# Kernel optimization log

Hardware: AMD Instinct MI355X
Metric: run time of the kernel (lower is better)

Reference implementation:

```python
import jax, jax.numpy as jnp
from jax import lax
import numpy as np

B, H, W, C, N = 4, 512, 512, 32, 300000
K, S, P, D = 3, 2, 1, 1  # kernel, stride, padding, dilation


def setup_inputs() -> dict:
    key = jax.random.key(0)
    kf, _ = jax.random.split(key)
    features = jax.random.normal(kf, (N, C), dtype=jnp.float32)
    # unique active coordinates (spconv requires unique sites)
    rng = np.random.default_rng(0)
    lin = rng.choice(B * H * W, size=N, replace=False)
    b = lin // (H * W)
    y = (lin // W) % H
    x = lin % W
    coors = jnp.asarray(np.stack([b, y, x], axis=1), dtype=jnp.int32)  # [N,3]
    return {"features": features, "coors": coors, "batch_size": B}


def reference(features, coors, batch_size):
    # Scatter active features onto a dense grid initialized to -inf so that
    # inputs only; outputs with no active input in window are inactive).
    neg_inf = jnp.array(-jnp.inf, dtype=features.dtype)
    dense = jnp.full((batch_size, H, W, features.shape[1]), neg_inf,
                     dtype=features.dtype)
    b, y, x = coors[:, 0], coors[:, 1], coors[:, 2]
    dense = dense.at[b, y, x].set(features)  # coords are unique
    out = lax.reduce_window(
        dense, neg_inf, lax.max,
        window_dimensions=(1, K, K, 1),
        window_strides=(1, S, S, 1),
        padding=((0, 0), (P, P), (P, P), (0, 0)),
        window_dilation=(1, D, D, 1))
    # inactive output sites -> 0 (dense view of the sparse output tensor)
    return jnp.where(jnp.isinf(out), jnp.zeros((), out.dtype), out)
```

## Files before the change

kernel.cpp:

```cpp
#include <hip/hip_runtime.h>
#include <math.h>

#define BB 4
#define HH 512
#define WW 512
#define CC 32
#define HO 256
#define WO 256

__global__ void fill_zero_kernel(int4* __restrict__ g, int n4) {
    int i = blockIdx.x * blockDim.x + threadIdx.x;
    if (i < n4) g[i] = make_int4(0, 0, 0, 0);
}

__global__ void scatter_idx_kernel(const int* __restrict__ coors,
                                   int* __restrict__ grid, int n) {
    int i = blockIdx.x * blockDim.x + threadIdx.x;
    if (i >= n) return;
    int b = coors[i * 3 + 0];
    int y = coors[i * 3 + 1];
    int x = coors[i * 3 + 2];
    grid[((size_t)b * HH + y) * WW + x] = i + 1;
}

__global__ void __launch_bounds__(256)
pool_kernel(const float4* __restrict__ feat,
            const int* __restrict__ grid,
            float4* __restrict__ out) {
    int ox_base = (blockIdx.x & 7) * 32;
    int oy      = (blockIdx.x >> 3) & (HO - 1);
    int b       = blockIdx.x >> 11;

    int tid = threadIdx.x;
    int cg  = tid & 7;
    int p   = tid >> 3;

    int iy0 = 2 * oy - 1;
    int gx0 = 2 * ox_base - 1;
    const int* gb = grid + (size_t)b * (HH * WW);

    __shared__ int sg[3 * 66];

    if (tid < 195) {
        int r = tid / 65;
        int c = tid - r * 65;
        int iy = iy0 + r;
        int gx = gx0 + c;
        int v = 0;
        if ((unsigned)iy < (unsigned)HH && (unsigned)gx < (unsigned)WW)
            v = gb[iy * WW + gx];
        sg[r * 66 + c] = v;
    }
    __syncthreads();

    const float NEG = -INFINITY;
    float4 acc = make_float4(NEG, NEG, NEG, NEG);
    int lc = 2 * p;

#pragma unroll
    for (int dy = 0; dy < 3; ++dy) {
#pragma unroll
        for (int dx = 0; dx < 3; ++dx) {
            int v = sg[dy * 66 + lc + dx];
            if (v != 0) {
                float4 f = feat[(size_t)(v - 1) * 8 + cg];
                acc.x = fmaxf(acc.x, f.x);
                acc.y = fmaxf(acc.y, f.y);
                acc.z = fmaxf(acc.z, f.z);
                acc.w = fmaxf(acc.w, f.w);
            }
        }
    }

    acc.x = isinf(acc.x) ? 0.0f : acc.x;
    acc.y = isinf(acc.y) ? 0.0f : acc.y;
    acc.z = isinf(acc.z) ? 0.0f : acc.z;
    acc.w = isinf(acc.w) ? 0.0f : acc.w;

    int pos = ((b * HO + oy) * WO + ox_base + p);
    out[(size_t)pos * 8 + cg] = acc;
}

extern "C" void kernel_launch(void* const* d_in, const int* in_sizes, int n_in,
                              void* d_out, int out_size, void* d_ws, size_t ws_size,
                              hipStream_t stream) {
    const float* features = (const float*)d_in[0];
    const int*   coors    = (const int*)d_in[1];
    int n = in_sizes[0] / CC;

    int* grid = (int*)d_ws;

    {
        int n4 = (BB * HH * WW) / 4;
        int blk = 256, grd = (n4 + blk - 1) / blk;
        fill_zero_kernel<<<grd, blk, 0, stream>>>((int4*)grid, n4);
    }
    {
        int blk = 256, grd = (n + blk - 1) / blk;
        scatter_idx_kernel<<<grd, blk, 0, stream>>>(coors, grid, n);
    }
    {
        int grd = BB * HO * (WO / 32);
        pool_kernel<<<grd, 256, 0, stream>>>((const float4*)features, grid,
                                             (float4*)d_out);
    }
}
```

Before: 114.2 us.

## Compact active sites per block and stage their features in shared memory

The pool kernel now compacts the nonzero grid entries of each block's 3x65 input window with a wave ballot and a shared atomic counter. It loads each active site's feature row once into bank-swizzled shared memory, so the columns shared by neighbouring output windows are no longer fetched from global memory repeatedly. If more than MAXOCC sites are active the code falls back to direct global loads. The change adds two extra barriers and about 12KB of shared memory per block, and raises the launch bounds hint to 8 blocks per CU.

Result: faster. 107.0 us (-6.3%).

```diff
diff --git a/kernel.cpp b/kernel.cpp
--- a/kernel.cpp
+++ b/kernel.cpp
@@ -7,6 +7,8 @@
 #define CC 32
 #define HO 256
 #define WO 256
+
+#define MAXOCC 96
 
 __global__ void fill_zero_kernel(int4* __restrict__ g, int n4) {
     int i = blockIdx.x * blockDim.x + threadIdx.x;
@@ -23,7 +25,7 @@
     grid[((size_t)b * HH + y) * WW + x] = i + 1;
 }
 
-__global__ void __launch_bounds__(256)
+__global__ void __launch_bounds__(256, 8)
 pool_kernel(const float4* __restrict__ feat,
             const int* __restrict__ grid,
             float4* __restrict__ out) {
@@ -31,45 +33,85 @@
     int oy      = (blockIdx.x >> 3) & (HO - 1);
     int b       = blockIdx.x >> 11;
 
-    int tid = threadIdx.x;
-    int cg  = tid & 7;
-    int p   = tid >> 3;
+    int tid  = threadIdx.x;
+    int lane = tid & 63;
+    int cg   = tid & 7;
+    int p    = tid >> 3;
 
     int iy0 = 2 * oy - 1;
     int gx0 = 2 * ox_base - 1;
     const int* gb = grid + (size_t)b * (HH * WW);
 
-    __shared__ int sg[3 * 66];
+    __shared__ int    cnt;
+    __shared__ int    smap[3 * 65];
+    __shared__ int    srcidx[MAXOCC];
+    __shared__ float4 sfeat[MAXOCC * 8];
 
-    if (tid < 195) {
-        int r = tid / 65;
-        int c = tid - r * 65;
-        int iy = iy0 + r;
-        int gx = gx0 + c;
+    if (tid == 0) cnt = 0;
+    __syncthreads();
+
+    {
         int v = 0;
-        if ((unsigned)iy < (unsigned)HH && (unsigned)gx < (unsigned)WW)
-            v = gb[iy * WW + gx];
-        sg[r * 66 + c] = v;
+        if (tid < 195) {
+            int r = tid / 65;
+            int c = tid - r * 65;
+            int iy = iy0 + r;
+            int gx = gx0 + c;
+            if ((unsigned)iy < (unsigned)HH && (unsigned)gx < (unsigned)WW)
+                v = gb[iy * WW + gx];
+        }
+        unsigned long long mask = __ballot(v != 0);
+        int nz = (int)__popcll(mask);
+        int base = 0;
+        if (lane == 0 && nz) base = atomicAdd(&cnt, nz);
+        base = __shfl(base, 0);
+        int prefix = (int)__popcll(mask & ((1ull << lane) - 1ull));
+        if (tid < 195) {
+            int m = 0;
+            if (v != 0) {
+                int s = base + prefix;
+                if (s < MAXOCC) { srcidx[s] = v - 1; m = s + 1; }
+                else            { m = -v; }
+            }
+            smap[tid] = m;
+        }
     }
     __syncthreads();
 
+    int total = cnt < MAXOCC ? cnt : MAXOCC;
+    for (int s = (tid >> 3); s < total; s += 32)
+        sfeat[(s << 3) + ((cg + s) & 7)] = feat[(size_t)srcidx[s] * 8 + cg];
+    __syncthreads();
+
+    int lc = 2 * p;
     const float NEG = -INFINITY;
     float4 acc = make_float4(NEG, NEG, NEG, NEG);
-    int lc = 2 * p;
-
 #pragma unroll
-    for (int dy = 0; dy < 3; ++dy) {
-#pragma unroll
-        for (int dx = 0; dx < 3; ++dx) {
-            int v = sg[dy * 66 + lc + dx];
-            if (v != 0) {
-                float4 f = feat[(size_t)(v - 1) * 8 + cg];
-                acc.x = fmaxf(acc.x, f.x);
-                acc.y = fmaxf(acc.y, f.y);
-                acc.z = fmaxf(acc.z, f.z);
-                acc.w = fmaxf(acc.w, f.w);
-            }
-        }
+    for (int r = 0; r < 3; ++r) {
+        int m0 = smap[r * 65 + lc + 0];
+        int m1 = smap[r * 65 + lc + 1];
+        int m2 = smap[r * 65 + lc + 2];
+        int s0 = m0 > 0 ? m0 - 1 : 0;
+        int s1 = m1 > 0 ? m1 - 1 : 0;
+        int s2 = m2 > 0 ? m2 - 1 : 0;
+        float4 f0 = sfeat[(s0 << 3) + ((cg + s0) & 7)];
+        float4 f1 = sfeat[(s1 << 3) + ((cg + s1) & 7)];
+        float4 f2 = sfeat[(s2 << 3) + ((cg + s2) & 7)];
+        if (m0 < 0) f0 = feat[(size_t)(-m0 - 1) * 8 + cg];
+        if (m1 < 0) f1 = feat[(size_t)(-m1 - 1) * 8 + cg];
+        if (m2 < 0) f2 = feat[(size_t)(-m2 - 1) * 8 + cg];
+        acc.x = fmaxf(acc.x, m0 != 0 ? f0.x : NEG);
+        acc.y = fmaxf(acc.y, m0 != 0 ? f0.y : NEG);
+        acc.z = fmaxf(acc.z, m0 != 0 ? f0.z : NEG);
+        acc.w = fmaxf(acc.w, m0 != 0 ? f0.w : NEG);
+        acc.x = fmaxf(acc.x, m1 != 0 ? f1.x : NEG);
+        acc.y = fmaxf(acc.y, m1 != 0 ? f1.y : NEG);
+        acc.z = fmaxf(acc.z, m1 != 0 ? f1.z : NEG);
+        acc.w = fmaxf(acc.w, m1 != 0 ? f1.w : NEG);
+        acc.x = fmaxf(acc.x, m2 != 0 ? f2.x : NEG);
+        acc.y = fmaxf(acc.y, m2 != 0 ? f2.y : NEG);
+        acc.z = fmaxf(acc.z, m2 != 0 ? f2.z : NEG);
+        acc.w = fmaxf(acc.w, m2 != 0 ? f2.w : NEG);
     }
 
     acc.x = isinf(acc.x) ? 0.0f : acc.x;
@@ -77,8 +119,8 @@
     acc.z = isinf(acc.z) ? 0.0f : acc.z;
     acc.w = isinf(acc.w) ? 0.0f : acc.w;
 
-    int pos = ((b * HO + oy) * WO + ox_base + p);
-    out[(size_t)pos * 8 + cg] = acc;
+    size_t pos = ((size_t)(b * HO + oy) * WO + ox_base + p);
+    out[pos * 8 + cg] = acc;
 }
 
 extern "C" void kernel_launch(void* const* d_in, const int* in_sizes, int n_in,
```
